# Kernel tuning notes

Measured on AMD Instinct MI355X. Metric: run time of the kernel, lower is better.

The kernel has to match this reference:

```python
import jax, jax.numpy as jnp
import numpy as np

H = 16  # number of heads (init kwarg h)

def vdp_matmul(a, va, b, vb):
    # VDP propagation through a matmul of two independent Gaussian tensors:
    # mean = a @ b ; var = va @ vb + va @ b^2 + a^2 @ vb
    mu = jnp.matmul(a, b)
    var = jnp.matmul(va, vb) + jnp.matmul(va, b * b) + jnp.matmul(a * a, vb)
    return mu, var

def softmax_vdp(a, va):
    # diagonal-Jacobian VDP softmax: p = softmax(a); var = (p(1-p))^2 * va
    p = jax.nn.softmax(a, axis=-1)
    return p, (p * (1.0 - p)) ** 2 * va

def setup_inputs() -> dict:
    key = jax.random.key(0)
    ks = jax.random.split(key, 8)
    B, S, D = 2, 1024, 1024
    sc = 1.0 / np.sqrt(D)
    return {
        "x": jax.random.normal(ks[0], (B, S, D), jnp.float32),
        "var_x": jax.random.uniform(ks[1], (B, S, D), jnp.float32) * 0.1,
        "wq_mu": jax.random.normal(ks[2], (D, D), jnp.float32) * sc,
        "wq_var": jax.random.uniform(ks[3], (D, D), jnp.float32) * 0.01,
        "wk_mu": jax.random.normal(ks[4], (D, D), jnp.float32) * sc,
        "wk_var": jax.random.uniform(ks[5], (D, D), jnp.float32) * 0.01,
        "wv_mu": jax.random.normal(ks[6], (D, D), jnp.float32) * sc,
        "wv_var": jax.random.uniform(ks[7], (D, D), jnp.float32) * 0.01,
    }

def _split_heads(t, h):
    B, S, D = t.shape
    return t.reshape(B, S, h, D // h).transpose(0, 2, 1, 3)  # [B,h,S,dh]

def reference(x, var_x, wq_mu, wq_var, wk_mu, wk_var, wv_mu, wv_var):
    D = x.shape[-1]
    rd = jnp.sqrt(jnp.asarray(D, x.dtype))
    # LinearVDP (bias=False): treat weight^T as the second VDP matmul operand
    q, vq = vdp_matmul(x, var_x, wq_mu.T, wq_var.T)
    k, vk = vdp_matmul(x, var_x, wk_mu.T, wk_var.T)
    v, vv = vdp_matmul(x, var_x, wv_mu.T, wv_var.T)
    q, vq = _split_heads(q, H), _split_heads(vq, H)
    k, vk = _split_heads(k, H), _split_heads(vk, H)
    v, vv = _split_heads(v, H), _split_heads(vv, H)
    # scores: q @ k^T with VDP variance, scaled (masking=False path)
    a, va = vdp_matmul(q, vq, k.transpose(0, 1, 3, 2), vk.transpose(0, 1, 3, 2))
    a, va = a / rd, va / (rd * rd)
    a, va = softmax_vdp(a, va)
    # attention-weighted values with VDP variance
    a, va = vdp_matmul(a, va, v, vv)
    a = a.transpose(0, 2, 1, 3).reshape(x.shape)      # [B,S,D]
    va = va.transpose(0, 2, 1, 3).reshape(x.shape)    # [B,S,D]
    return x + a, va
```

## Files before the change

kernel.cpp:

```cpp
#include <hip/hip_runtime.h>
#include <stdint.h>

typedef unsigned short u16;
typedef __attribute__((ext_vector_type(4))) float f32x4;
typedef __attribute__((ext_vector_type(8))) short s16x8;
typedef __attribute__((ext_vector_type(2))) unsigned u32x2;

#define MFMA16(a,b,c) __builtin_amdgcn_mfma_f32_16x16x32_bf16(a,b,c,0,0,0)

__device__ inline u16 f2b(float f){
  unsigned u = __float_as_uint(f);
  unsigned r = u + 0x7fffu + ((u>>16)&1u);
  return (u16)(r>>16);
}
__device__ inline float b2f(u16 b){
  return __uint_as_float(((unsigned)b)<<16);
}
__device__ inline unsigned cvtpk(float lo, float hi){
  unsigned r;
  asm("v_cvt_pk_bf16_f32 %0, %1, %2" : "=v"(r) : "v"(lo), "v"(hi));
  return r;
}
__device__ inline void load_lds16(const void* g, void* l){
  __builtin_amdgcn_global_load_lds((const __attribute__((address_space(1))) void*)g,
                                   (__attribute__((address_space(3))) void*)l, 16, 0, 0);
}

__global__ void prep_x_kernel(const float* __restrict__ x, const float* __restrict__ vx,
                              u16* __restrict__ xb, u16* __restrict__ acat){
  int i = blockIdx.x*256 + threadIdx.x;
  int m = i >> 10, j = i & 1023;
  float xv = x[i];
  xb[i] = f2b(xv);
  size_t ar = (size_t)m*2048;
  acat[ar + j]        = f2b(vx[i]);
  acat[ar + 1024 + j] = f2b(xv*xv);
}

__global__ void prep_w_kernel(const float* __restrict__ w0mu, const float* __restrict__ w0va,
                              const float* __restrict__ w1mu, const float* __restrict__ w1va,
                              const float* __restrict__ w2mu, const float* __restrict__ w2va,
                              u16* __restrict__ wmub, u16* __restrict__ bcat){
  int z = blockIdx.z;
  const float* wmu = z==0?w0mu:(z==1?w1mu:w2mu);
  const float* wva = z==0?w0va:(z==1?w1va:w2va);
  u16* wb = wmub + (size_t)z*1048576;
  u16* bc = bcat + (size_t)z*2097152;
  int i = blockIdx.x*256 + threadIdx.x;
  int n = i >> 10, j = i & 1023;
  float mu = wmu[i], va = wva[i];
  wb[i] = f2b(mu);
  size_t br = (size_t)n*2048;
  bc[br + j]        = f2b(va + mu*mu);
  bc[br + 1024 + j] = f2b(va);
}

__global__ void prep_mid_kernel(const u16* __restrict__ qb, const u16* __restrict__ kb,
                                const u16* __restrict__ vkb,
                                u16* __restrict__ kw2, u16* __restrict__ qsq){
  int i = blockIdx.x*256 + threadIdx.x;
  float kk = b2f(kb[i]);
  float vk = b2f(vkb[i]);
  kw2[i] = f2b(vk + kk*kk);
  float q = b2f(qb[i]);
  qsq[i] = f2b(q*q);
}

__global__ void transpose3_kernel(const u16* __restrict__ vb, const u16* __restrict__ vvb,
                                  u16* __restrict__ vT, u16* __restrict__ vw2T,
                                  u16* __restrict__ vvT){
  int z = blockIdx.z;
  u16* out = z==0?vT:(z==1?vw2T:vvT);
  __shared__ u16 t[32][33];
  int tx = threadIdx.x & 31, ty = threadIdx.x >> 5;
  int c0 = blockIdx.x*32, r0 = blockIdx.y*32;
  #pragma unroll
  for (int rr=0; rr<32; rr+=8){
    size_t idx = (size_t)(r0+ty+rr)*1024 + c0+tx;
    u16 val;
    if (z==0)      val = vb[idx];
    else if (z==2) val = vvb[idx];
    else {
      float v  = b2f(vb[idx]);
      float vv = b2f(vvb[idx]);
      val = f2b(vv + v*v);
    }
    t[ty+rr][tx] = val;
  }
  __syncthreads();
  #pragma unroll
  for (int rr=0; rr<32; rr+=8)
    out[(size_t)(c0+ty+rr)*2048 + r0+tx] = t[tx][ty+rr];
}

__global__ __launch_bounds__(256) void gemm_nt6_kernel(
    const u16* __restrict__ xb, const u16* __restrict__ acat,
    const u16* __restrict__ wmub, const u16* __restrict__ bcat,
    u16* __restrict__ cbase, int N){
  int z = blockIdx.z;
  const u16* A = z<3 ? xb : acat;
  int K = z<3 ? 1024 : 2048;
  const u16* B = z<3 ? wmub + (size_t)z*1048576 : bcat + (size_t)(z-3)*2097152;
  u16* C = cbase + (size_t)z*2097152;
  __shared__ __align__(16) u16 As[128*32];
  __shared__ __align__(16) u16 Bs[128*32];
  int tid = threadIdx.x;
  int wid = tid>>6, lane = tid&63;
  int wr = wid>>1, wc = wid&1;
  int fr = lane&15, kg = lane>>4;
  int m0 = blockIdx.x*128, n0 = blockIdx.y*128;
  int srow = lane>>2;
  int scol = (lane&3)*8;
  f32x4 acc[4][4] = {};
  for (int k0=0; k0<K; k0+=32){
    #pragma unroll
    for (int c=0;c<2;c++){
      int r = c*64 + wid*16 + srow;
      load_lds16(A + (size_t)(m0+r)*K + k0 + scol, (char*)As + (size_t)(c*64+wid*16)*64);
      load_lds16(B + (size_t)(n0+r)*K + k0 + scol, (char*)Bs + (size_t)(c*64+wid*16)*64);
    }
    __syncthreads();
    s16x8 af[4], bfv[4];
    #pragma unroll
    for (int i=0;i<4;i++){
      af[i]  = *(const s16x8*)(As + (wr*64 + i*16 + fr)*32 + kg*8);
      bfv[i] = *(const s16x8*)(Bs + (wc*64 + i*16 + fr)*32 + kg*8);
    }
    #pragma unroll
    for (int i=0;i<4;i++)
      #pragma unroll
      for (int j=0;j<4;j++)
        acc[i][j] = MFMA16(af[i], bfv[j], acc[i][j]);
    __syncthreads();
  }
  #pragma unroll
  for (int i=0;i<4;i++)
    #pragma unroll
    for (int j=0;j<4;j++)
      #pragma unroll
      for (int r=0;r<4;r++){
        int row = m0 + wr*64 + i*16 + kg*4 + r;
        int col = n0 + wc*64 + j*16 + fr;
        C[(size_t)row*N + col] = f2b(acc[i][j][r]);
      }
}

__global__ __launch_bounds__(256) void attn_vdp_kernel(
  const u16* __restrict__ qb, const u16* __restrict__ vqb, const u16* __restrict__ qsq,
  const u16* __restrict__ kb, const u16* __restrict__ kw2, const u16* __restrict__ vkb,
  const u16* __restrict__ vT, const u16* __restrict__ vw2T, const u16* __restrict__ vvT,
  const float* __restrict__ x, float* __restrict__ out0, float* __restrict__ out1){
  int qblk = blockIdx.x, h = blockIdx.y, b = blockIdx.z;
  int wid = threadIdx.x>>6, lane = threadIdx.x&63;
  int fr = lane&15, kg = lane>>4;
  int qrow0 = qblk*64 + wid*16;
  size_t mbase = (size_t)b*1024;

  __shared__ __align__(16) u16 bufA[3][4096];
  __shared__ __align__(16) u16 bufB[3][4096];
  __shared__ __align__(16) u16 plds[4][3][16][72];

  const int srow = lane>>3;
  const int sci  = (lane&7) ^ srow;
  const int c0   = wid*2;

  auto stA1 = [&](int jt, u16* dst){
    size_t base = (mbase + (size_t)jt*64)*1024 + h*64;
    #pragma unroll
    for (int c2=0;c2<2;c2++){
      int c = c0+c2;
      size_t go = base + (size_t)(c*8+srow)*1024 + sci*8;
      load_lds16(kb + go, (char*)dst + c*1024);
    }
  };
  auto stK3 = [&](int jt){
    size_t base = (mbase + (size_t)jt*64)*1024 + h*64;
    #pragma unroll
    for (int c2=0;c2<2;c2++){
      int c = c0+c2;
      size_t go = base + (size_t)(c*8+srow)*1024 + sci*8;
      load_lds16(kb  + go, (char*)bufA[0] + c*1024);
      load_lds16(kw2 + go, (char*)bufA[1] + c*1024);
      load_lds16(vkb + go, (char*)bufA[2] + c*1024);
    }
  };
  auto stV3 = [&](int jt){
    size_t base = (size_t)(h*64)*2048 + mbase + (size_t)jt*64;
    #pragma unroll
    for (int c2=0;c2<2;c2++){
      int c = c0+c2;
      size_t go = base + (size_t)(c*8+srow)*2048 + sci*8;
      load_lds16(vT   + go, (char*)bufB[0] + c*1024);
      load_lds16(vw2T + go, (char*)bufB[1] + c*1024);
      load_lds16(vvT  + go, (char*)bufB[2] + c*1024);
    }
  };
  auto frag = [&](const u16* t, int ni, int kf)->s16x8{
    int R = ni*16+fr;
    return *(const s16x8*)(t + R*64 + (((kg + kf*4) ^ (R&7))<<3));
  };

  s16x8 qa[2], vqa[2], qsa[2];
  {
    size_t ro = (mbase + qrow0 + fr)*1024 + h*64 + kg*8;
    #pragma unroll
    for (int kf=0;kf<2;kf++){
      qa[kf]  = *(const s16x8*)(qb  + ro + kf*32);
      vqa[kf] = *(const s16x8*)(vqb + ro + kf*32);
      qsa[kf] = *(const s16x8*)(qsq + ro + kf*32);
    }
  }
  const float scale = 0.03125f;

  float lsum = 0.f;
  stA1(0, bufA[0]);
  __syncthreads();
  for (int jt=0;jt<16;jt++){
    const u16* cur = (jt&1) ? bufB[0] : bufA[0];
    if (jt<15) stA1(jt+1, (jt&1) ? bufA[0] : bufB[0]);
    else       stK3(0);
    f32x4 sacc[4] = {};
    #pragma unroll
    for (int ni=0;ni<4;ni++)
      #pragma unroll
      for (int kf=0;kf<2;kf++)
        sacc[ni] = MFMA16(frag(cur,ni,kf), qa[kf], sacc[ni]);
    #pragma unroll
    for (int ni=0;ni<4;ni++)
      #pragma unroll
      for (int r=0;r<4;r++)
        lsum += __expf(sacc[ni][r]*scale);
    __syncthreads();
  }
  lsum += __shfl_xor(lsum, 16);
  lsum += __shfl_xor(lsum, 32);
  const float linv = 1.f/lsum;

  f32x4 omu[4] = {}, ova[4] = {};
  for (int jt=0;jt<16;jt++){
    stV3(jt);
    f32x4 sacc[4] = {}, vacc[4] = {};
    #pragma unroll
    for (int ni=0;ni<4;ni++)
      #pragma unroll
      for (int kf=0;kf<2;kf++){
        sacc[ni] = MFMA16(frag(bufA[0],ni,kf), qa[kf],  sacc[ni]);
        vacc[ni] = MFMA16(frag(bufA[1],ni,kf), vqa[kf], vacc[ni]);
        vacc[ni] = MFMA16(frag(bufA[2],ni,kf), qsa[kf], vacc[ni]);
      }
    #pragma unroll
    for (int ni=0;ni<4;ni++){
      float pv[4], vpv[4], psv[4];
      #pragma unroll
      for (int r=0;r<4;r++){
        float p  = __expf(sacc[ni][r]*scale) * linv;
        float va = vacc[ni][r] * 9.765625e-4f;
        float g  = p*(1.f-p);
        pv[r]  = p;
        vpv[r] = g*g*va;
        psv[r] = p*p;
      }
      *(u32x2*)&plds[wid][0][fr][ni*16+kg*4] = (u32x2){cvtpk(pv[0],pv[1]),   cvtpk(pv[2],pv[3])};
      *(u32x2*)&plds[wid][1][fr][ni*16+kg*4] = (u32x2){cvtpk(vpv[0],vpv[1]), cvtpk(vpv[2],vpv[3])};
      *(u32x2*)&plds[wid][2][fr][ni*16+kg*4] = (u32x2){cvtpk(psv[0],psv[1]), cvtpk(psv[2],psv[3])};
    }
    s16x8 pa[2], vpa[2], pqa[2];
    #pragma unroll
    for (int kf=0;kf<2;kf++){
      pa[kf]  = *(const s16x8*)&plds[wid][0][fr][kf*32 + kg*8];
      vpa[kf] = *(const s16x8*)&plds[wid][1][fr][kf*32 + kg*8];
      pqa[kf] = *(const s16x8*)&plds[wid][2][fr][kf*32 + kg*8];
    }
    __syncthreads();
    if (jt<15) stK3(jt+1);
    #pragma unroll
    for (int ni=0;ni<4;ni++)
      #pragma unroll
      for (int kf=0;kf<2;kf++){
        omu[ni] = MFMA16(pa[kf],  frag(bufB[0],ni,kf), omu[ni]);
        ova[ni] = MFMA16(vpa[kf], frag(bufB[1],ni,kf), ova[ni]);
        ova[ni] = MFMA16(pqa[kf], frag(bufB[2],ni,kf), ova[ni]);
      }
    __syncthreads();
  }

  #pragma unroll
  for (int ni=0;ni<4;ni++){
    #pragma unroll
    for (int r=0;r<4;r++){
      size_t idx = (mbase + qrow0 + kg*4 + r)*1024 + h*64 + ni*16 + fr;
      out0[idx] = x[idx] + omu[ni][r];
      out1[idx] = ova[ni][r];
    }
  }
}

extern "C" void kernel_launch(void* const* d_in, const int* in_sizes, int n_in,
                              void* d_out, int out_size, void* d_ws, size_t ws_size,
                              hipStream_t stream){
  const float* x    = (const float*)d_in[0];
  const float* vx   = (const float*)d_in[1];
  const float* wqmu = (const float*)d_in[2];
  const float* wqva = (const float*)d_in[3];
  const float* wkmu = (const float*)d_in[4];
  const float* wkva = (const float*)d_in[5];
  const float* wvmu = (const float*)d_in[6];
  const float* wvva = (const float*)d_in[7];
  float* out0 = (float*)d_out;
  float* out1 = out0 + 2u*1024u*1024u;

  char* w = (char*)d_ws;
  const size_t MB = 1024*1024;
  u16* xb   = (u16*)(w +  0*MB);
  u16* acat = (u16*)(w +  4*MB);
  u16* wmub = (u16*)(w + 12*MB);
  u16* bcat = (u16*)(w + 18*MB);
  u16* qb_  = (u16*)(w + 30*MB);
  u16* kb_  = (u16*)(w + 34*MB);
  u16* vb_  = (u16*)(w + 38*MB);
  u16* vqb  = (u16*)(w + 42*MB);
  u16* vkb  = (u16*)(w + 46*MB);
  u16* vvb  = (u16*)(w + 50*MB);
  u16* kw2  = (u16*)(w + 54*MB);
  u16* qsq  = (u16*)(w + 58*MB);
  u16* vT   = (u16*)(w + 62*MB);
  u16* vw2T = (u16*)(w + 66*MB);
  u16* vvT  = (u16*)(w + 70*MB);

  prep_x_kernel<<<8192, 256, 0, stream>>>(x, vx, xb, acat);
  prep_w_kernel<<<dim3(4096,1,3), 256, 0, stream>>>(wqmu,wqva,wkmu,wkva,wvmu,wvva,
                                                    wmub, bcat);
  gemm_nt6_kernel<<<dim3(16,8,6), 256, 0, stream>>>(xb, acat, wmub, bcat, qb_, 1024);
  prep_mid_kernel<<<8192, 256, 0, stream>>>(qb_, kb_, vkb, kw2, qsq);
  transpose3_kernel<<<dim3(32,64,3), 256, 0, stream>>>(vb_, vvb, vT, vw2T, vvT);
  attn_vdp_kernel<<<dim3(16,16,2), 256, 0, stream>>>(qb_, vqb, qsq, kb_, kw2, vkb,
                                                     vT, vw2T, vvT, x, out0, out1);
}
```

Baseline: 222.8 us.

## Merge prep kernels, widen GEMM K-tile with swizzled LDS, compute q^2 in attention

Folds the x and weight prep kernels into one launch, and the k-variance prep and V transposes into another. The standalone q-squared buffer is removed; q^2 is now computed in registers inside the attention kernel. The projection GEMM moves to a 64-wide K tile with XOR-swizzled LDS, uses a flattened grid that interleaves the six GEMMs, swaps the MFMA operands, and stores packed bf16 pairs instead of scalar u16 writes. The aim is fewer launches, less memory traffic and fewer LDS bank conflicts, at the cost of twice the LDS per GEMM block.

```diff
diff --git a/kernel.cpp b/kernel.cpp
--- a/kernel.cpp
+++ b/kernel.cpp
@@ -26,127 +26,141 @@
                                    (__attribute__((address_space(3))) void*)l, 16, 0, 0);
 }
 
-__global__ void prep_x_kernel(const float* __restrict__ x, const float* __restrict__ vx,
-                              u16* __restrict__ xb, u16* __restrict__ acat){
-  int i = blockIdx.x*256 + threadIdx.x;
-  int m = i >> 10, j = i & 1023;
-  float xv = x[i];
-  xb[i] = f2b(xv);
-  size_t ar = (size_t)m*2048;
-  acat[ar + j]        = f2b(vx[i]);
-  acat[ar + 1024 + j] = f2b(xv*xv);
-}
-
-__global__ void prep_w_kernel(const float* __restrict__ w0mu, const float* __restrict__ w0va,
-                              const float* __restrict__ w1mu, const float* __restrict__ w1va,
-                              const float* __restrict__ w2mu, const float* __restrict__ w2va,
-                              u16* __restrict__ wmub, u16* __restrict__ bcat){
-  int z = blockIdx.z;
-  const float* wmu = z==0?w0mu:(z==1?w1mu:w2mu);
-  const float* wva = z==0?w0va:(z==1?w1va:w2va);
-  u16* wb = wmub + (size_t)z*1048576;
-  u16* bc = bcat + (size_t)z*2097152;
-  int i = blockIdx.x*256 + threadIdx.x;
-  int n = i >> 10, j = i & 1023;
-  float mu = wmu[i], va = wva[i];
-  wb[i] = f2b(mu);
-  size_t br = (size_t)n*2048;
-  bc[br + j]        = f2b(va + mu*mu);
-  bc[br + 1024 + j] = f2b(va);
-}
-
-__global__ void prep_mid_kernel(const u16* __restrict__ qb, const u16* __restrict__ kb,
-                                const u16* __restrict__ vkb,
-                                u16* __restrict__ kw2, u16* __restrict__ qsq){
-  int i = blockIdx.x*256 + threadIdx.x;
-  float kk = b2f(kb[i]);
-  float vk = b2f(vkb[i]);
-  kw2[i] = f2b(vk + kk*kk);
-  float q = b2f(qb[i]);
-  qsq[i] = f2b(q*q);
-}
-
-__global__ void transpose3_kernel(const u16* __restrict__ vb, const u16* __restrict__ vvb,
-                                  u16* __restrict__ vT, u16* __restrict__ vw2T,
-                                  u16* __restrict__ vvT){
-  int z = blockIdx.z;
-  u16* out = z==0?vT:(z==1?vw2T:vvT);
-  __shared__ u16 t[32][33];
-  int tx = threadIdx.x & 31, ty = threadIdx.x >> 5;
-  int c0 = blockIdx.x*32, r0 = blockIdx.y*32;
-  #pragma unroll
-  for (int rr=0; rr<32; rr+=8){
-    size_t idx = (size_t)(r0+ty+rr)*1024 + c0+tx;
-    u16 val;
-    if (z==0)      val = vb[idx];
-    else if (z==2) val = vvb[idx];
-    else {
-      float v  = b2f(vb[idx]);
-      float vv = b2f(vvb[idx]);
-      val = f2b(vv + v*v);
-    }
-    t[ty+rr][tx] = val;
-  }
-  __syncthreads();
-  #pragma unroll
-  for (int rr=0; rr<32; rr+=8)
-    out[(size_t)(c0+ty+rr)*2048 + r0+tx] = t[tx][ty+rr];
+__global__ void prep_in_kernel(const float* __restrict__ x, const float* __restrict__ vx,
+                               const float* __restrict__ w0mu, const float* __restrict__ w0va,
+                               const float* __restrict__ w1mu, const float* __restrict__ w1va,
+                               const float* __restrict__ w2mu, const float* __restrict__ w2va,
+                               u16* __restrict__ xb, u16* __restrict__ acat,
+                               u16* __restrict__ wmub, u16* __restrict__ bcat){
+  int bid = blockIdx.x;
+  if (bid < 8192){
+    int i = bid*256 + threadIdx.x;
+    int j = i & 1023;
+    float xv = x[i];
+    xb[i] = f2b(xv);
+    size_t ar = (size_t)(i >> 10)*2048;
+    acat[ar + j]        = f2b(vx[i]);
+    acat[ar + 1024 + j] = f2b(xv*xv);
+  } else {
+    int t = bid - 8192;
+    int z = t >> 12;
+    int i = (t & 4095)*256 + threadIdx.x;
+    const float* wmu = z==0?w0mu:(z==1?w1mu:w2mu);
+    const float* wva = z==0?w0va:(z==1?w1va:w2va);
+    u16* wb = wmub + (size_t)z*1048576;
+    u16* bc = bcat + (size_t)z*2097152;
+    int j = i & 1023;
+    float mu = wmu[i], va = wva[i];
+    wb[i] = f2b(mu);
+    size_t br = (size_t)(i >> 10)*2048;
+    bc[br + j]        = f2b(va + mu*mu);
+    bc[br + 1024 + j] = f2b(va);
+  }
 }
 
 __global__ __launch_bounds__(256) void gemm_nt6_kernel(
     const u16* __restrict__ xb, const u16* __restrict__ acat,
     const u16* __restrict__ wmub, const u16* __restrict__ bcat,
-    u16* __restrict__ cbase, int N){
-  int z = blockIdx.z;
+    u16* __restrict__ cbase){
+  int bid = blockIdx.x;
+  int z = bid % 6;
+  int xy = bid / 6;
+  int bx = xy & 15, by = xy >> 4;
   const u16* A = z<3 ? xb : acat;
   int K = z<3 ? 1024 : 2048;
   const u16* B = z<3 ? wmub + (size_t)z*1048576 : bcat + (size_t)(z-3)*2097152;
   u16* C = cbase + (size_t)z*2097152;
-  __shared__ __align__(16) u16 As[128*32];
-  __shared__ __align__(16) u16 Bs[128*32];
+  const int N = 1024;
+  __shared__ __align__(16) u16 As[128*64];
+  __shared__ __align__(16) u16 Bs[128*64];
   int tid = threadIdx.x;
   int wid = tid>>6, lane = tid&63;
   int wr = wid>>1, wc = wid&1;
   int fr = lane&15, kg = lane>>4;
-  int m0 = blockIdx.x*128, n0 = blockIdx.y*128;
-  int srow = lane>>2;
-  int scol = (lane&3)*8;
+  int m0 = bx*128, n0 = by*128;
+  int srow = lane>>3;
+  int sci  = (lane&7) ^ srow;
   f32x4 acc[4][4] = {};
-  for (int k0=0; k0<K; k0+=32){
-    #pragma unroll
-    for (int c=0;c<2;c++){
-      int r = c*64 + wid*16 + srow;
-      load_lds16(A + (size_t)(m0+r)*K + k0 + scol, (char*)As + (size_t)(c*64+wid*16)*64);
-      load_lds16(B + (size_t)(n0+r)*K + k0 + scol, (char*)Bs + (size_t)(c*64+wid*16)*64);
-    }
-    __syncthreads();
-    s16x8 af[4], bfv[4];
-    #pragma unroll
-    for (int i=0;i<4;i++){
-      af[i]  = *(const s16x8*)(As + (wr*64 + i*16 + fr)*32 + kg*8);
-      bfv[i] = *(const s16x8*)(Bs + (wc*64 + i*16 + fr)*32 + kg*8);
-    }
-    #pragma unroll
-    for (int i=0;i<4;i++)
-      #pragma unroll
-      for (int j=0;j<4;j++)
-        acc[i][j] = MFMA16(af[i], bfv[j], acc[i][j]);
+  for (int k0=0; k0<K; k0+=64){
+    #pragma unroll
+    for (int cc=0; cc<4; cc++){
+      int c = wid*4 + cc;
+      size_t gra = (size_t)(m0 + c*8 + srow)*K + k0 + sci*8;
+      size_t grb = (size_t)(n0 + c*8 + srow)*K + k0 + sci*8;
+      load_lds16(A + gra, (char*)As + c*1024);
+      load_lds16(B + grb, (char*)Bs + c*1024);
+    }
+    __syncthreads();
+    #pragma unroll
+    for (int kf=0;kf<2;kf++){
+      s16x8 af[4], bfv[4];
+      #pragma unroll
+      for (int i=0;i<4;i++){
+        int Ra = wr*64 + i*16 + fr;
+        int Rb = wc*64 + i*16 + fr;
+        af[i]  = *(const s16x8*)(As + Ra*64 + (((kg + kf*4) ^ (Ra&7))<<3));
+        bfv[i] = *(const s16x8*)(Bs + Rb*64 + (((kg + kf*4) ^ (Rb&7))<<3));
+      }
+      #pragma unroll
+      for (int i=0;i<4;i++)
+        #pragma unroll
+        for (int j=0;j<4;j++)
+          acc[i][j] = MFMA16(bfv[j], af[i], acc[i][j]);
+    }
     __syncthreads();
   }
   #pragma unroll
-  for (int i=0;i<4;i++)
-    #pragma unroll
-    for (int j=0;j<4;j++)
-      #pragma unroll
-      for (int r=0;r<4;r++){
-        int row = m0 + wr*64 + i*16 + kg*4 + r;
-        int col = n0 + wc*64 + j*16 + fr;
-        C[(size_t)row*N + col] = f2b(acc[i][j][r]);
-      }
+  for (int i=0;i<4;i++){
+    int mrow = m0 + wr*64 + i*16 + fr;
+    #pragma unroll
+    for (int j=0;j<4;j++){
+      int ncol = n0 + wc*64 + j*16 + kg*4;
+      u32x2 pk = {cvtpk(acc[i][j][0],acc[i][j][1]), cvtpk(acc[i][j][2],acc[i][j][3])};
+      *(u32x2*)(C + (size_t)mrow*N + ncol) = pk;
+    }
+  }
+}
+
+__global__ void mid_kernel(const u16* __restrict__ kb, const u16* __restrict__ vkb,
+                           u16* __restrict__ kw2,
+                           const u16* __restrict__ vb, const u16* __restrict__ vvb,
+                           u16* __restrict__ vT, u16* __restrict__ vw2T,
+                           u16* __restrict__ vvT){
+  __shared__ u16 t[32][33];
+  int bid = blockIdx.x;
+  if (bid < 6144){
+    int z = bid / 2048, wI = bid % 2048;
+    int bx = wI & 31, by = wI >> 5;
+    u16* out = z==0?vT:(z==1?vw2T:vvT);
+    int tx = threadIdx.x & 31, ty = threadIdx.x >> 5;
+    int c0 = bx*32, r0 = by*32;
+    #pragma unroll
+    for (int rr=0; rr<32; rr+=8){
+      size_t idx = (size_t)(r0+ty+rr)*1024 + c0+tx;
+      u16 val;
+      if (z==0)      val = vb[idx];
+      else if (z==2) val = vvb[idx];
+      else {
+        float v  = b2f(vb[idx]);
+        float vv = b2f(vvb[idx]);
+        val = f2b(vv + v*v);
+      }
+      t[ty+rr][tx] = val;
+    }
+    __syncthreads();
+    #pragma unroll
+    for (int rr=0; rr<32; rr+=8)
+      out[(size_t)(c0+ty+rr)*2048 + r0+tx] = t[tx][ty+rr];
+  } else {
+    int i = (bid - 6144)*256 + threadIdx.x;
+    float kk = b2f(kb[i]);
+    float vk = b2f(vkb[i]);
+    kw2[i] = f2b(vk + kk*kk);
+  }
 }
 
 __global__ __launch_bounds__(256) void attn_vdp_kernel(
-  const u16* __restrict__ qb, const u16* __restrict__ vqb, const u16* __restrict__ qsq,
+  const u16* __restrict__ qb, const u16* __restrict__ vqb,
   const u16* __restrict__ kb, const u16* __restrict__ kw2, const u16* __restrict__ vkb,
   const u16* __restrict__ vT, const u16* __restrict__ vw2T, const u16* __restrict__ vvT,
   const float* __restrict__ x, float* __restrict__ out0, float* __restrict__ out1){
@@ -207,7 +221,14 @@
     for (int kf=0;kf<2;kf++){
       qa[kf]  = *(const s16x8*)(qb  + ro + kf*32);
       vqa[kf] = *(const s16x8*)(vqb + ro + kf*32);
-      qsa[kf] = *(const s16x8*)(qsq + ro + kf*32);
+      #pragma unroll
+      for (int e=0;e<8;e+=2){
+        float lo = b2f((u16)qa[kf][e]);
+        float hi = b2f((u16)qa[kf][e+1]);
+        unsigned pk = cvtpk(lo*lo, hi*hi);
+        qsa[kf][e]   = (short)(pk & 0xffffu);
+        qsa[kf][e+1] = (short)(pk >> 16);
+      }
     }
   }
   const float scale = 0.03125f;
@@ -322,17 +343,14 @@
   u16* vkb  = (u16*)(w + 46*MB);
   u16* vvb  = (u16*)(w + 50*MB);
   u16* kw2  = (u16*)(w + 54*MB);
-  u16* qsq  = (u16*)(w + 58*MB);
-  u16* vT   = (u16*)(w + 62*MB);
-  u16* vw2T = (u16*)(w + 66*MB);
-  u16* vvT  = (u16*)(w + 70*MB);
-
-  prep_x_kernel<<<8192, 256, 0, stream>>>(x, vx, xb, acat);
-  prep_w_kernel<<<dim3(4096,1,3), 256, 0, stream>>>(wqmu,wqva,wkmu,wkva,wvmu,wvva,
-                                                    wmub, bcat);
-  gemm_nt6_kernel<<<dim3(16,8,6), 256, 0, stream>>>(xb, acat, wmub, bcat, qb_, 1024);
-  prep_mid_kernel<<<8192, 256, 0, stream>>>(qb_, kb_, vkb, kw2, qsq);
-  transpose3_kernel<<<dim3(32,64,3), 256, 0, stream>>>(vb_, vvb, vT, vw2T, vvT);
-  attn_vdp_kernel<<<dim3(16,16,2), 256, 0, stream>>>(qb_, vqb, qsq, kb_, kw2, vkb,
+  u16* vT   = (u16*)(w + 58*MB);
+  u16* vw2T = (u16*)(w + 62*MB);
+  u16* vvT  = (u16*)(w + 66*MB);
+
+  prep_in_kernel<<<20480, 256, 0, stream>>>(x, vx, wqmu, wqva, wkmu, wkva, wvmu, wvva,
+                                            xb, acat, wmub, bcat);
+  gemm_nt6_kernel<<<768, 256, 0, stream>>>(xb, acat, wmub, bcat, qb_);
+  mid_kernel<<<14336, 256, 0, stream>>>(kb_, vkb, kw2, vb_, vvb, vT, vw2T, vvT);
+  attn_vdp_kernel<<<dim3(16,16,2), 256, 0, stream>>>(qb_, vqb, kb_, kw2, vkb,
                                                      vT, vw2T, vvT, x, out0, out1);
 }
```

After: 239.2 us. 1.07x slower.
